# Kernel tuning notes

Hardware: AMD Instinct MI355X
Metric: run time of the kernel (lower is better)

## Reference

```python
import jax, jax.numpy as jnp
import numpy as np

B, S, H, E, K = 4, 4096, 2048, 64, 2
LN_EPS = 1e-5
AUX_EPS = 1e-9


def setup_inputs() -> dict:
    key = jax.random.key(0)
    ks = jax.random.split(key, 5)
    lim1 = 1.0 / np.sqrt(H)
    x = jax.random.normal(ks[0], (B, S, H), dtype=jnp.float32)
    W1 = jax.random.uniform(ks[1], (H, H), jnp.float32, -lim1, lim1)
    b1 = jax.random.uniform(ks[2], (H,), jnp.float32, -lim1, lim1)
    W2 = jax.random.uniform(ks[3], (H, E), jnp.float32, -lim1, lim1)
    b2 = jax.random.uniform(ks[4], (E,), jnp.float32, -lim1, lim1)
    gamma = jnp.ones((H,), jnp.float32)
    beta = jnp.zeros((H,), jnp.float32)
    return {"x": x, "W1": W1, "b1": b1, "W2": W2, "b2": b2, "gamma": gamma, "beta": beta}


def reference(x, W1, b1, W2, b2, gamma, beta):
    # LayerNorm over hidden dim
    mu = jnp.mean(x, axis=-1, keepdims=True)
    var = jnp.mean(jnp.square(x - mu), axis=-1, keepdims=True)
    x_norm = (x - mu) * jax.lax.rsqrt(var + LN_EPS) * gamma + beta
    # 2-layer router MLP: Linear -> ReLU -> Linear
    h = jax.nn.relu(jnp.einsum('bsh,hk->bsk', x_norm, W1) + b1)
    logits = jnp.einsum('bsh,he->bse', h, W2) + b2  # [B,S,E]
    probs = jax.nn.softmax(logits, axis=-1)
    # top-k + renormalize
    top_k_probs, top_k_indices = jax.lax.top_k(probs, K)
    top_k_probs = top_k_probs / jnp.sum(top_k_probs, axis=-1, keepdims=True)
    # aux load-balancing loss
    p_expert = jnp.mean(probs, axis=(0, 1))  # [E]
    aux_loss = jnp.sum(p_expert * jnp.log(p_expert * E + AUX_EPS))
    return top_k_indices, top_k_probs, aux_loss
```

## Files before the change

### kernel.cpp

```cpp
#include <hip/hip_runtime.h>
#include <hip/hip_fp16.h>
#include <cstdint>
#include <cstddef>

#define HH   2048
#define MM   16384
#define NE   64
#define FIXCAP 3072
#define MARGIN 1.0e-3f
#define LN_EPS  1e-5f
#define AUX_EPS 1e-9f

typedef __attribute__((ext_vector_type(8))) _Float16 f16x8;
typedef __attribute__((ext_vector_type(4))) _Float16 f16x4;
typedef __attribute__((ext_vector_type(4))) float    f32x4;

__device__ __forceinline__ void gload_lds16(const void* g, void* l) {
    __builtin_amdgcn_global_load_lds(
        (const __attribute__((address_space(1))) unsigned int*)g,
        (__attribute__((address_space(3))) unsigned int*)l,
        16, 0, 0);
}

__device__ __forceinline__ uint32_t swz64(uint32_t x) {
    return x ^ (((x >> 7) & 3u) << 4) ^ (((x >> 9) & 1u) << 6);
}
__device__ __forceinline__ uint32_t swz128(uint32_t x) {
    return x ^ (((x >> 8) & 7u) << 4);
}

__global__ __launch_bounds__(256) void k_tw1(const float* __restrict__ W1,
                                             _Float16* __restrict__ whp,
                                             _Float16* __restrict__ wlp) {
    __shared__ float tile[32][33];
    int tx = threadIdx.x & 31;
    int ty = threadIdx.x >> 5;
    int bx = blockIdx.x & 63;
    int by = blockIdx.x >> 6;
#pragma unroll
    for (int i = 0; i < 4; ++i) {
        int k = by * 32 + ty + i * 8;
        tile[ty + i * 8][tx] = W1[(size_t)k * HH + bx * 32 + tx];
    }
    __syncthreads();
#pragma unroll
    for (int i = 0; i < 4; ++i) {
        int n = bx * 32 + ty + i * 8;
        float w = tile[tx][ty + i * 8];
        _Float16 hi = (_Float16)w;
        _Float16 lo = (_Float16)((w - (float)hi) * 1024.0f);
        whp[(size_t)n * HH + by * 32 + tx] = hi;
        wlp[(size_t)n * HH + by * 32 + tx] = lo;
    }
}

__global__ __launch_bounds__(256) void k_w2q(const float* __restrict__ W2,
                                             _Float16* __restrict__ w2q) {
    int e = blockIdx.x;
    int t = threadIdx.x;
#pragma unroll
    for (int j = 0; j < 8; ++j) {
        int c = t * 8 + j;
        float w = W2[(size_t)c * NE + e];
        _Float16 hi = (_Float16)w;
        _Float16 lo = (_Float16)((w - (float)hi) * 1024.0f);
        f16x4 q = {hi, hi, lo, (_Float16)0.0f};
        *(f16x4*)&w2q[(size_t)e * 8192 + (size_t)c * 4] = q;
    }
}

__global__ __launch_bounds__(256) void k_ln(const float* __restrict__ x,
                                            const float* __restrict__ gamma,
                                            const float* __restrict__ beta,
                                            _Float16* __restrict__ xh,
                                            _Float16* __restrict__ xl) {
    int row = blockIdx.x;
    int t = threadIdx.x;
    const float4* xr = (const float4*)(x + (size_t)row * HH);
    float4 v0 = xr[t];
    float4 v1 = xr[t + 256];
    float s  = v0.x + v0.y + v0.z + v0.w + v1.x + v1.y + v1.z + v1.w;
    float sq = v0.x*v0.x + v0.y*v0.y + v0.z*v0.z + v0.w*v0.w
             + v1.x*v1.x + v1.y*v1.y + v1.z*v1.z + v1.w*v1.w;
#pragma unroll
    for (int m = 1; m < 64; m <<= 1) { s += __shfl_xor(s, m); sq += __shfl_xor(sq, m); }
    __shared__ float red[8];
    int wv = t >> 6;
    if ((t & 63) == 0) { red[wv] = s; red[wv + 4] = sq; }
    __syncthreads();
    s  = red[0] + red[1] + red[2] + red[3];
    sq = red[4] + red[5] + red[6] + red[7];
    float mu  = s * (1.0f / HH);
    float var = sq * (1.0f / HH) - mu * mu;
    float rr  = rsqrtf(var + LN_EPS);

    const float4* gr = (const float4*)gamma;
    const float4* br = (const float4*)beta;
#pragma unroll
    for (int p = 0; p < 2; ++p) {
        int idx = t + p * 256;
        float4 v = (p == 0) ? v0 : v1;
        float4 g = gr[idx];
        float4 b = br[idx];
        float f[4];
        f[0] = (v.x - mu) * rr * g.x + b.x;
        f[1] = (v.y - mu) * rr * g.y + b.y;
        f[2] = (v.z - mu) * rr * g.z + b.z;
        f[3] = (v.w - mu) * rr * g.w + b.w;
        f16x4 oh, ol;
#pragma unroll
        for (int j = 0; j < 4; ++j) {
            _Float16 hi = (_Float16)f[j];
            oh[j] = hi;
            ol[j] = (_Float16)(f[j] - (float)hi);
        }
        *(f16x4*)&xh[(size_t)row * HH + idx * 4] = oh;
        *(f16x4*)&xl[(size_t)row * HH + idx * 4] = ol;
    }
}

#define VMW0 do { asm volatile("s_waitcnt vmcnt(0)" ::: "memory"); \
                  __builtin_amdgcn_sched_barrier(0); } while (0)

#define STAGE1(IT) do { uint32_t kb = (uint32_t)(IT) * 128;                    \
    char* dst = lds + (((IT) & 1) << 16);                                      \
    gload_lds16(pxh + gA0 + kb,      dst + dstb0);                             \
    gload_lds16(pxh + gA1 + kb,      dst + dstb1);                             \
    gload_lds16(pxh + gA0 + kb + 64, dst + 16384 + dstb0);                     \
    gload_lds16(pxh + gA1 + kb + 64, dst + 16384 + dstb1);                     \
    gload_lds16(pwh + gB0 + kb,      dst + 32768 + dstb0);                     \
    gload_lds16(pwh + gB1 + kb,      dst + 32768 + dstb1);                     \
    gload_lds16(pwh + gB0 + kb + 64, dst + 49152 + dstb0);                     \
    gload_lds16(pwh + gB1 + kb + 64, dst + 49152 + dstb1);                     \
} while (0)

__global__ __launch_bounds__(512, 2) void k_gemm1(const _Float16* __restrict__ Ah_g,
                                                  const _Float16* __restrict__ Bh_g,
                                                  const _Float16* __restrict__ w2q,
                                                  const float* __restrict__ b1,
                                                  float* __restrict__ part) {
    __shared__ __align__(16) char lds[131072];

    int xcd = blockIdx.x & 7;
    int idx = blockIdx.x >> 3;
    int bm  = xcd * 8 + (idx >> 3);
    int bn  = idx & 7;
    int t = threadIdx.x;
    int lane = t & 63;
    int wid = t >> 6;
    int wm = wid >> 2;
    int wn = wid & 3;
    int r16 = lane & 15, ko = lane >> 4;

    f32x4 acc[8][4];
#pragma unroll
    for (int m = 0; m < 8; ++m)
#pragma unroll
        for (int n = 0; n < 4; ++n)
            acc[m][n] = (f32x4){0.f, 0.f, 0.f, 0.f};

    const char* pxh = (const char*)Ah_g;
    const char* pwh = (const char*)Bh_g;

    uint32_t dstb0 = (uint32_t)t * 16;
    uint32_t dstb1 = 8192 + dstb0;
    uint32_t L0 = swz64(dstb0), L1 = swz64(dstb1);
    uint32_t gA0 = ((uint32_t)bm * 256 + (L0 >> 6)) * (HH * 2) + (L0 & 63);
    uint32_t gA1 = ((uint32_t)bm * 256 + (L1 >> 6)) * (HH * 2) + (L1 & 63);
    uint32_t gB0 = ((uint32_t)bn * 256 + (L0 >> 6)) * (HH * 2) + (L0 & 63);
    uint32_t gB1 = ((uint32_t)bn * 256 + (L1 >> 6)) * (HH * 2) + (L1 & 63);

    uint32_t aoff[8], boff[4];
#pragma unroll
    for (int m = 0; m < 8; ++m)
        aoff[m] = swz64((uint32_t)(wm * 128 + m * 16 + r16) * 64 + ko * 16);
#pragma unroll
    for (int n = 0; n < 4; ++n)
        boff[n] = swz64((uint32_t)(wn * 64 + n * 16 + r16) * 64 + ko * 16);

    STAGE1(0);
    VMW0;
    __builtin_amdgcn_s_barrier();

    for (int it = 0; it < 32; ++it) {
        char* slot = lds + ((it & 1) << 16);
#pragma unroll
        for (int sub = 0; sub < 2; ++sub) {
            const char* Axh = slot + sub * 16384;
            const char* Bwh = slot + 32768 + sub * 16384;
            f16x8 fbh[4], fah[4];
#pragma unroll
            for (int n = 0; n < 4; ++n) fbh[n] = *(const f16x8*)(Bwh + boff[n]);
#pragma unroll
            for (int m = 0; m < 4; ++m) fah[m] = *(const f16x8*)(Axh + aoff[m]);
            if (sub == 0 && it < 31) STAGE1(it + 1);
            __builtin_amdgcn_s_setprio(1);
#pragma unroll
            for (int m = 0; m < 4; ++m)
#pragma unroll
                for (int n = 0; n < 4; ++n)
                    acc[m][n] = __builtin_amdgcn_mfma_f32_16x16x32_f16(fah[m], fbh[n], acc[m][n], 0, 0, 0);
            __builtin_amdgcn_s_setprio(0);
#pragma unroll
            for (int m = 0; m < 4; ++m) fah[m] = *(const f16x8*)(Axh + aoff[4 + m]);
            __builtin_amdgcn_s_setprio(1);
#pragma unroll
            for (int m = 0; m < 4; ++m)
#pragma unroll
                for (int n = 0; n < 4; ++n)
                    acc[4 + m][n] = __builtin_amdgcn_mfma_f32_16x16x32_f16(fah[m], fbh[n], acc[4 + m][n], 0, 0, 0);
            __builtin_amdgcn_s_setprio(0);
        }
        if (it < 31) VMW0;
        __builtin_amdgcn_s_barrier();
    }

    char* A2 = lds;
    char* B2 = lds + 32768;

    float bv[4];
#pragma unroll
    for (int n = 0; n < 4; ++n)
        bv[n] = b1[bn * 256 + wn * 64 + n * 16 + r16];

    f32x4 acc2[2][4];
#pragma unroll
    for (int mf = 0; mf < 2; ++mf)
#pragma unroll
        for (int ef = 0; ef < 4; ++ef)
            acc2[mf][ef] = (f32x4){0.f, 0.f, 0.f, 0.f};

    int hi4 = lane >> 4;
    int ko16 = ko * 16;

#pragma unroll
    for (int c = 0; c < 16; ++c) {
        {
            int e = t >> 3;
            int cb = (t & 7) * 16;
            const char* src = (const char*)w2q + (size_t)e * 16384
                            + (size_t)bn * 2048 + (size_t)c * 128 + cb;
            *(f16x8*)(B2 + swz128((uint32_t)e * 128 + cb)) = *(const f16x8*)src;
        }
        if (wn == (c >> 2)) {
            const int n = c & 3;
#pragma unroll
            for (int m = 0; m < 8; ++m)
#pragma unroll
                for (int i = 0; i < 4; ++i) {
                    float h = acc[m][n][i] + bv[n];
                    h = fmaxf(h, 0.f);
                    _Float16 hh = (_Float16)h;
                    float hhf = (float)hh;
                    _Float16 hl = (_Float16)(h - hhf);
                    _Float16 hs = (_Float16)(hhf * 0.0009765625f);
                    int row = wm * 128 + m * 16 + hi4 * 4 + i;
                    f16x4 q = {hh, hl, hs, (_Float16)0.0f};
                    *(f16x4*)(A2 + swz128((uint32_t)row * 128 + r16 * 8)) = q;
                }
        }
        __syncthreads();
#pragma unroll
        for (int kk = 0; kk < 2; ++kk) {
            f16x8 bfr[4];
#pragma unroll
            for (int ef = 0; ef < 4; ++ef)
                bfr[ef] = *(const f16x8*)(B2 +
                    swz128((uint32_t)(ef * 16 + r16) * 128 + kk * 64 + ko16));
#pragma unroll
            for (int mf = 0; mf < 2; ++mf) {
                f16x8 afr = *(const f16x8*)(A2 +
                    swz128((uint32_t)(wid * 32 + mf * 16 + r16) * 128 + kk * 64 + ko16));
#pragma unroll
                for (int ef = 0; ef < 4; ++ef)
                    acc2[mf][ef] = __builtin_amdgcn_mfma_f32_16x16x32_f16(
                        afr, bfr[ef], acc2[mf][ef], 0, 0, 0);
            }
        }
        __syncthreads();
    }

#pragma unroll
    for (int mf = 0; mf < 2; ++mf)
#pragma unroll
        for (int i = 0; i < 4; ++i) {
            int grow = bm * 256 + wid * 32 + mf * 16 + hi4 * 4 + i;
            float* dst = part + ((size_t)bn * MM + grow) * NE;
#pragma unroll
            for (int ef = 0; ef < 4; ++ef)
                dst[ef * 16 + r16] = acc2[mf][ef][i];
        }
}

__global__ __launch_bounds__(64) void k_screen(const float* __restrict__ part,
                                               const float* __restrict__ b2,
                                               float* __restrict__ out,
                                               float* __restrict__ sums,
                                               int* __restrict__ list,
                                               int* __restrict__ cnt) {
    int lane = threadIdx.x;
    int r = blockIdx.x * 64 + lane;
    float l[NE];
#pragma unroll
    for (int e = 0; e < NE; e += 4) {
        float4 b = *(const float4*)&b2[e];
        l[e] = b.x; l[e + 1] = b.y; l[e + 2] = b.z; l[e + 3] = b.w;
    }
    for (int sl = 0; sl < 8; ++sl) {
        const float* ps = part + ((size_t)sl * MM + r) * NE;
#pragma unroll
        for (int e = 0; e < NE; e += 4) {
            float4 v = *(const float4*)&ps[e];
            l[e] += v.x; l[e + 1] += v.y; l[e + 2] += v.z; l[e + 3] += v.w;
        }
    }
    float m1 = -1e30f, m2 = -1e30f, m3 = -1e30f;
    int i1 = 0, i2 = 0;
#pragma unroll
    for (int e = 0; e < NE; ++e) {
        if (l[e] > m1)      { m3 = m2; m2 = m1; i2 = i1; m1 = l[e]; i1 = e; }
        else if (l[e] > m2) { m3 = m2; m2 = l[e]; i2 = e; }
        else if (l[e] > m3) { m3 = l[e]; }
    }
    float ev[NE];
    float Z = 0.f;
#pragma unroll
    for (int e = 0; e < NE; ++e) { ev[e] = expf(l[e] - m1); Z += ev[e]; }

    float eb = expf(m2 - m1);
    float pa = 1.0f / (1.0f + eb);
    float pb = eb * pa;

    out[(size_t)r * 2 + 0] = (float)i1;
    out[(size_t)r * 2 + 1] = (float)i2;
    out[(size_t)2 * MM + r * 2 + 0] = pa;
    out[(size_t)2 * MM + r * 2 + 1] = pb;

    if ((m1 - m2 < MARGIN) || (m2 - m3 < MARGIN)) {
        int s = atomicAdd(cnt, 1);
        if (s < FIXCAP) list[s] = r;
    }

    float invZ = 1.0f / Z;
    float keep = 0.f;
#pragma unroll
    for (int e = 0; e < NE; ++e) {
        float q = ev[e] * invZ;
#pragma unroll
        for (int sh = 1; sh < 64; sh <<= 1) q += __shfl_xor(q, sh);
        if (lane == e) keep = q;
    }
    atomicAdd(&sums[lane], keep);
}

#define STAGEF_A(KT) do { uint32_t kb = (uint32_t)(KT) * 64;                   \
    char* dst = lds + (((KT) & 1) << 16);                                      \
    gload_lds16(pxh + gA0 + kb, dst + dstb0);                                  \
    gload_lds16(pxh + gA1 + kb, dst + dstb1);                                  \
    gload_lds16(pxl + gA0 + kb, dst + 16384 + dstb0);                          \
    gload_lds16(pxl + gA1 + kb, dst + 16384 + dstb1);                          \
} while (0)

#define STAGEF_B(KT) do { uint32_t kb = (uint32_t)(KT) * 64;                   \
    char* dst = lds + (((KT) & 1) << 16) + 32768;                              \
    gload_lds16(pwh + gB0 + kb, dst + dstb0);                                  \
    gload_lds16(pwh + gB1 + kb, dst + dstb1);                                  \
    gload_lds16(pwl + gB0 + kb, dst + 16384 + dstb0);                          \
    gload_lds16(pwl + gB1 + kb, dst + 16384 + dstb1);                          \
} while (0)

__global__ __launch_bounds__(512, 2) void k_fixg(const _Float16* __restrict__ Ah_g,
                                                 const _Float16* __restrict__ Al_g,
                                                 const _Float16* __restrict__ Bh_g,
                                                 const _Float16* __restrict__ Bl_g,
                                                 const int* __restrict__ list,
                                                 const int* __restrict__ cnt,
                                                 float* __restrict__ hpart) {
    int ks = blockIdx.x & 3;
    int bn = (blockIdx.x >> 2) & 7;
    int bm = blockIdx.x >> 5;
    int cv = *cnt; if (cv > FIXCAP) cv = FIXCAP;
    if (bm * 256 >= cv) return;

    __shared__ __align__(16) char lds[131072];
    int t = threadIdx.x;
    int lane = t & 63;
    int wid = t >> 6;
    int wm = wid >> 2;
    int wn = wid & 3;
    int r16 = lane & 15, ko = lane >> 4;

    f32x4 acc[8][4];
#pragma unroll
    for (int m = 0; m < 8; ++m)
#pragma unroll
        for (int n = 0; n < 4; ++n)
            acc[m][n] = (f32x4){0.f, 0.f, 0.f, 0.f};

    const char* pxh = (const char*)Ah_g;
    const char* pxl = (const char*)Al_g;
    const char* pwh = (const char*)Bh_g;
    const char* pwl = (const char*)Bl_g;

    uint32_t dstb0 = (uint32_t)t * 16;
    uint32_t dstb1 = 8192 + dstb0;
    uint32_t L0 = swz64(dstb0), L1 = swz64(dstb1);
    int rA0 = list[bm * 256 + (L0 >> 6)];
    int rA1 = list[bm * 256 + (L1 >> 6)];
    uint32_t kso = (uint32_t)ks * 1024;
    uint32_t gA0 = (uint32_t)rA0 * (HH * 2) + (L0 & 63) + kso;
    uint32_t gA1 = (uint32_t)rA1 * (HH * 2) + (L1 & 63) + kso;
    uint32_t gB0 = ((uint32_t)bn * 256 + (L0 >> 6)) * (HH * 2) + (L0 & 63) + kso;
    uint32_t gB1 = ((uint32_t)bn * 256 + (L1 >> 6)) * (HH * 2) + (L1 & 63) + kso;

    uint32_t aoff[8], boff[4];
#pragma unroll
    for (int m = 0; m < 8; ++m)
        aoff[m] = swz64((uint32_t)(wm * 128 + m * 16 + r16) * 64 + ko * 16);
#pragma unroll
    for (int n = 0; n < 4; ++n)
        boff[n] = swz64((uint32_t)(wn * 64 + n * 16 + r16) * 64 + ko * 16);

    STAGEF_A(0);
    STAGEF_B(0);
    VMW0;
    __builtin_amdgcn_s_barrier();

    for (int kt = 0; kt < 16; ++kt) {
        char* slot = lds + ((kt & 1) << 16);
        const char* Axh = slot;
        const char* Axl = slot + 16384;
        const char* Bwh = slot + 32768;
        const char* Bwl = slot + 49152;

        f16x8 fbh[4], fbl[4], fah[4], fal[4];
#pragma unroll
        for (int n = 0; n < 4; ++n) {
            fbh[n] = *(const f16x8*)(Bwh + boff[n]);
            fbl[n] = *(const f16x8*)(Bwl + boff[n]);
        }
#pragma unroll
        for (int m = 0; m < 4; ++m) {
            fah[m] = *(const f16x8*)(Axh + aoff[m]);
            fal[m] = *(const f16x8*)(Axl + aoff[m]);
        }
        if (kt < 15) STAGEF_A(kt + 1);
        __builtin_amdgcn_s_setprio(1);
#pragma unroll
        for (int m = 0; m < 4; ++m) {
            f16x8 fas = fah[m] * (_Float16)0.0009765625f;
#pragma unroll
            for (int n = 0; n < 4; ++n) {
                acc[m][n] = __builtin_amdgcn_mfma_f32_16x16x32_f16(fah[m], fbh[n], acc[m][n], 0, 0, 0);
                acc[m][n] = __builtin_amdgcn_mfma_f32_16x16x32_f16(fal[m], fbh[n], acc[m][n], 0, 0, 0);
                acc[m][n] = __builtin_amdgcn_mfma_f32_16x16x32_f16(fas,    fbl[n], acc[m][n], 0, 0, 0);
            }
        }
        __builtin_amdgcn_s_setprio(0);

#pragma unroll
        for (int m = 0; m < 4; ++m) {
            fah[m] = *(const f16x8*)(Axh + aoff[4 + m]);
            fal[m] = *(const f16x8*)(Axl + aoff[4 + m]);
        }
        if (kt < 15) STAGEF_B(kt + 1);
        __builtin_amdgcn_s_setprio(1);
#pragma unroll
        for (int m = 0; m < 4; ++m) {
            f16x8 fas = fah[m] * (_Float16)0.0009765625f;
#pragma unroll
            for (int n = 0; n < 4; ++n) {
                acc[4 + m][n] = __builtin_amdgcn_mfma_f32_16x16x32_f16(fah[m], fbh[n], acc[4 + m][n], 0, 0, 0);
                acc[4 + m][n] = __builtin_amdgcn_mfma_f32_16x16x32_f16(fal[m], fbh[n], acc[4 + m][n], 0, 0, 0);
                acc[4 + m][n] = __builtin_amdgcn_mfma_f32_16x16x32_f16(fas,    fbl[n], acc[4 + m][n], 0, 0, 0);
            }
        }
        __builtin_amdgcn_s_setprio(0);
        if (kt < 15) VMW0;
        __builtin_amdgcn_s_barrier();
    }

    float* hp = hpart + (size_t)ks * FIXCAP * HH;
    int hi4 = lane >> 4;
#pragma unroll
    for (int m = 0; m < 8; ++m)
#pragma unroll
        for (int n = 0; n < 4; ++n)
#pragma unroll
            for (int i = 0; i < 4; ++i) {
                int row_l = bm * 256 + wm * 128 + m * 16 + hi4 * 4 + i;
                int col = bn * 256 + wn * 64 + n * 16 + r16;
                hp[(size_t)row_l * HH + col] = acc[m][n][i];
            }
}

__global__ __launch_bounds__(256) void k_fix2(const float* __restrict__ hpart,
                                              const float* __restrict__ b1,
                                              const float* __restrict__ W2,
                                              const float* __restrict__ b2,
                                              const int* __restrict__ list,
                                              const int* __restrict__ cnt,
                                              float* __restrict__ out) {
    int n = *cnt; if (n > FIXCAP) n = FIXCAP;
    int gi = blockIdx.x;
    if (gi >= n) return;
    int r = list[gi];
    int e = threadIdx.x & 63;
    int kg = threadIdx.x >> 6;
    const float* h0 = hpart + (size_t)gi * HH;
    const float* h1 = h0 + (size_t)FIXCAP * HH;
    const float* h2 = h1 + (size_t)FIXCAP * HH;
    const float* h3 = h2 + (size_t)FIXCAP * HH;
    float p = 0.f;
    int k0 = kg * 512;
    for (int k = k0; k < k0 + 512; ++k) {
        float h = ((h0[k] + h1[k]) + (h2[k] + h3[k])) + b1[k];
        h = fmaxf(h, 0.f);
        p = fmaf(h, W2[(size_t)k * NE + e], p);
    }
    __shared__ float red[4][NE];
    red[kg][e] = p;
    __syncthreads();
    if (threadIdx.x < 64) {
        float l = ((red[0][e] + red[1][e]) + (red[2][e] + red[3][e])) + b2[e];
        float m1 = l;
#pragma unroll
        for (int sh = 1; sh < 64; sh <<= 1) m1 = fmaxf(m1, __shfl_xor(m1, sh));
        unsigned long long bb = __ballot(l == m1);
        int i1 = (int)(__ffsll((long long)bb) - 1);
        float l2 = (e == i1) ? -1e30f : l;
        float m2 = l2;
#pragma unroll
        for (int sh = 1; sh < 64; sh <<= 1) m2 = fmaxf(m2, __shfl_xor(m2, sh));
        unsigned long long bb2 = __ballot(l2 == m2);
        int i2 = (int)(__ffsll((long long)bb2) - 1);
        if (e == 0) {
            float eb = expf(m2 - m1);
            float pa = 1.0f / (1.0f + eb);
            float pb = eb * pa;
            out[(size_t)r * 2 + 0] = (float)i1;
            out[(size_t)r * 2 + 1] = (float)i2;
            out[(size_t)2 * MM + r * 2 + 0] = pa;
            out[(size_t)2 * MM + r * 2 + 1] = pb;
        }
    }
}

__global__ void k_aux(const float* __restrict__ sums, float* __restrict__ out) {
    if (threadIdx.x == 0) {
        float loss = 0.f;
        for (int e = 0; e < NE; ++e) {
            float p = sums[e] * (1.0f / MM);
            loss += p * logf(p * (float)NE + AUX_EPS);
        }
        out[(size_t)4 * MM] = loss;
    }
}

extern "C" void kernel_launch(void* const* d_in, const int* in_sizes, int n_in,
                              void* d_out, int out_size, void* d_ws, size_t ws_size,
                              hipStream_t stream) {
    const float* x     = (const float*)d_in[0];
    const float* W1    = (const float*)d_in[1];
    const float* b1    = (const float*)d_in[2];
    const float* W2    = (const float*)d_in[3];
    const float* b2    = (const float*)d_in[4];
    const float* gamma = (const float*)d_in[5];
    const float* beta  = (const float*)d_in[6];
    float* out = (float*)d_out;

    char* ws = (char*)d_ws;
    _Float16* xh   = (_Float16*)(ws);
    _Float16* xl   = (_Float16*)(ws + 67108864);
    _Float16* whp  = (_Float16*)(ws + 134217728);
    _Float16* wlp  = (_Float16*)(ws + 142606336);
    _Float16* w2q  = (_Float16*)(ws + 150994944);
    float*    part = (float*)   (ws + 152043520);
    float*   hpart = (float*)   (ws + 152043520);
    int*      list = (int*)     (ws + 252706816);
    float*    sums = (float*)   (ws + 252719104);
    int*      cnt  = (int*)     (ws + 252719360);

    hipMemsetAsync(sums, 0, 512, stream);
    hipMemsetAsync(list, 0, FIXCAP * 4, stream);
    k_tw1   <<<4096,    256, 0, stream>>>(W1, whp, wlp);
    k_w2q   <<<64,      256, 0, stream>>>(W2, w2q);
    k_ln    <<<MM,      256, 0, stream>>>(x, gamma, beta, xh, xl);
    k_gemm1 <<<512,     512, 0, stream>>>(xh, whp, w2q, b1, part);
    k_screen<<<MM/64,   64,  0, stream>>>(part, b2, out, sums, list, cnt);
    k_fixg  <<<384,     512, 0, stream>>>(xh, xl, whp, wlp, list, cnt, hpart);
    k_fix2  <<<FIXCAP,  256, 0, stream>>>(hpart, b1, W2, b2, list, cnt, out);
    k_aux   <<<1,       64,  0, stream>>>(sums, out);
}
```

Measured before the change: 367.7 us.

## Deepen GEMM1 LDS pipeline to four stages and use one wavefront per row in LayerNorm

The main GEMM loop moves from a double-buffered 128-wide K step to a four-slot ring of 64-wide K steps with three tiles in flight. It waits with partial vmcnt counts, so each step no longer has to fully drain outstanding loads before its barrier, which is meant to hide global-to-LDS latency better. Separately, the LayerNorm kernel now handles one row per wavefront, four rows per block, which drops the LDS reduction and block barrier. The trade-off is twice as many barriers in GEMM1 and more VGPRs in LayerNorm to hold eight float4 values per lane.

```diff
diff --git a/kernel.cpp b/kernel.cpp
--- a/kernel.cpp
+++ b/kernel.cpp
@@ -74,22 +74,19 @@
                                             const float* __restrict__ beta,
                                             _Float16* __restrict__ xh,
                                             _Float16* __restrict__ xl) {
-    int row = blockIdx.x;
-    int t = threadIdx.x;
+    int row = blockIdx.x * 4 + (threadIdx.x >> 6);
+    int lane = threadIdx.x & 63;
     const float4* xr = (const float4*)(x + (size_t)row * HH);
-    float4 v0 = xr[t];
-    float4 v1 = xr[t + 256];
-    float s  = v0.x + v0.y + v0.z + v0.w + v1.x + v1.y + v1.z + v1.w;
-    float sq = v0.x*v0.x + v0.y*v0.y + v0.z*v0.z + v0.w*v0.w
-             + v1.x*v1.x + v1.y*v1.y + v1.z*v1.z + v1.w*v1.w;
+    float4 v[8];
+    float s = 0.f, sq = 0.f;
+#pragma unroll
+    for (int j = 0; j < 8; ++j) {
+        v[j] = xr[lane + j * 64];
+        s  += v[j].x + v[j].y + v[j].z + v[j].w;
+        sq += v[j].x*v[j].x + v[j].y*v[j].y + v[j].z*v[j].z + v[j].w*v[j].w;
+    }
 #pragma unroll
     for (int m = 1; m < 64; m <<= 1) { s += __shfl_xor(s, m); sq += __shfl_xor(sq, m); }
-    __shared__ float red[8];
-    int wv = t >> 6;
-    if ((t & 63) == 0) { red[wv] = s; red[wv + 4] = sq; }
-    __syncthreads();
-    s  = red[0] + red[1] + red[2] + red[3];
-    sq = red[4] + red[5] + red[6] + red[7];
     float mu  = s * (1.0f / HH);
     float var = sq * (1.0f / HH) - mu * mu;
     float rr  = rsqrtf(var + LN_EPS);
@@ -97,41 +94,36 @@
     const float4* gr = (const float4*)gamma;
     const float4* br = (const float4*)beta;
 #pragma unroll
-    for (int p = 0; p < 2; ++p) {
-        int idx = t + p * 256;
-        float4 v = (p == 0) ? v0 : v1;
+    for (int j = 0; j < 8; ++j) {
+        int idx = lane + j * 64;
         float4 g = gr[idx];
         float4 b = br[idx];
         float f[4];
-        f[0] = (v.x - mu) * rr * g.x + b.x;
-        f[1] = (v.y - mu) * rr * g.y + b.y;
-        f[2] = (v.z - mu) * rr * g.z + b.z;
-        f[3] = (v.w - mu) * rr * g.w + b.w;
+        f[0] = (v[j].x - mu) * rr * g.x + b.x;
+        f[1] = (v[j].y - mu) * rr * g.y + b.y;
+        f[2] = (v[j].z - mu) * rr * g.z + b.z;
+        f[3] = (v[j].w - mu) * rr * g.w + b.w;
         f16x4 oh, ol;
 #pragma unroll
-        for (int j = 0; j < 4; ++j) {
-            _Float16 hi = (_Float16)f[j];
-            oh[j] = hi;
-            ol[j] = (_Float16)(f[j] - (float)hi);
+        for (int q = 0; q < 4; ++q) {
+            _Float16 hi = (_Float16)f[q];
+            oh[q] = hi;
+            ol[q] = (_Float16)(f[q] - (float)hi);
         }
         *(f16x4*)&xh[(size_t)row * HH + idx * 4] = oh;
         *(f16x4*)&xl[(size_t)row * HH + idx * 4] = ol;
     }
 }
 
-#define VMW0 do { asm volatile("s_waitcnt vmcnt(0)" ::: "memory"); \
-                  __builtin_amdgcn_sched_barrier(0); } while (0)
-
-#define STAGE1(IT) do { uint32_t kb = (uint32_t)(IT) * 128;                    \
-    char* dst = lds + (((IT) & 1) << 16);                                      \
-    gload_lds16(pxh + gA0 + kb,      dst + dstb0);                             \
-    gload_lds16(pxh + gA1 + kb,      dst + dstb1);                             \
-    gload_lds16(pxh + gA0 + kb + 64, dst + 16384 + dstb0);                     \
-    gload_lds16(pxh + gA1 + kb + 64, dst + 16384 + dstb1);                     \
-    gload_lds16(pwh + gB0 + kb,      dst + 32768 + dstb0);                     \
-    gload_lds16(pwh + gB1 + kb,      dst + 32768 + dstb1);                     \
-    gload_lds16(pwh + gB0 + kb + 64, dst + 49152 + dstb0);                     \
-    gload_lds16(pwh + gB1 + kb + 64, dst + 49152 + dstb1);                     \
+#define VMW(N) do { asm volatile("s_waitcnt vmcnt(" #N ")" ::: "memory"); \
+                    __builtin_amdgcn_sched_barrier(0); } while (0)
+
+#define STAGE1(KT) do { uint32_t kb = (uint32_t)(KT) * 64;                     \
+    char* dst = lds + (((KT) & 3) << 15);                                      \
+    gload_lds16(pxh + gA0 + kb, dst + dstb0);                                  \
+    gload_lds16(pxh + gA1 + kb, dst + dstb1);                                  \
+    gload_lds16(pwh + gB0 + kb, dst + 16384 + dstb0);                          \
+    gload_lds16(pwh + gB1 + kb, dst + 16384 + dstb1);                          \
 } while (0)
 
 __global__ __launch_bounds__(512, 2) void k_gemm1(const _Float16* __restrict__ Ah_g,
@@ -179,39 +171,41 @@
         boff[n] = swz64((uint32_t)(wn * 64 + n * 16 + r16) * 64 + ko * 16);
 
     STAGE1(0);
-    VMW0;
+    STAGE1(1);
+    STAGE1(2);
+    VMW(8);
     __builtin_amdgcn_s_barrier();
 
-    for (int it = 0; it < 32; ++it) {
-        char* slot = lds + ((it & 1) << 16);
-#pragma unroll
-        for (int sub = 0; sub < 2; ++sub) {
-            const char* Axh = slot + sub * 16384;
-            const char* Bwh = slot + 32768 + sub * 16384;
-            f16x8 fbh[4], fah[4];
-#pragma unroll
-            for (int n = 0; n < 4; ++n) fbh[n] = *(const f16x8*)(Bwh + boff[n]);
-#pragma unroll
-            for (int m = 0; m < 4; ++m) fah[m] = *(const f16x8*)(Axh + aoff[m]);
-            if (sub == 0 && it < 31) STAGE1(it + 1);
-            __builtin_amdgcn_s_setprio(1);
-#pragma unroll
-            for (int m = 0; m < 4; ++m)
-#pragma unroll
-                for (int n = 0; n < 4; ++n)
-                    acc[m][n] = __builtin_amdgcn_mfma_f32_16x16x32_f16(fah[m], fbh[n], acc[m][n], 0, 0, 0);
-            __builtin_amdgcn_s_setprio(0);
-#pragma unroll
-            for (int m = 0; m < 4; ++m) fah[m] = *(const f16x8*)(Axh + aoff[4 + m]);
-            __builtin_amdgcn_s_setprio(1);
-#pragma unroll
-            for (int m = 0; m < 4; ++m)
-#pragma unroll
-                for (int n = 0; n < 4; ++n)
-                    acc[4 + m][n] = __builtin_amdgcn_mfma_f32_16x16x32_f16(fah[m], fbh[n], acc[4 + m][n], 0, 0, 0);
-            __builtin_amdgcn_s_setprio(0);
-        }
-        if (it < 31) VMW0;
+    for (int kt = 0; kt < 64; ++kt) {
+        char* slot = lds + ((kt & 3) << 15);
+        const char* Axh = slot;
+        const char* Bwh = slot + 16384;
+
+        f16x8 fbh[4], fah[4];
+#pragma unroll
+        for (int n = 0; n < 4; ++n) fbh[n] = *(const f16x8*)(Bwh + boff[n]);
+#pragma unroll
+        for (int m = 0; m < 4; ++m) fah[m] = *(const f16x8*)(Axh + aoff[m]);
+        if (kt < 61) STAGE1(kt + 3);
+        __builtin_amdgcn_s_setprio(1);
+#pragma unroll
+        for (int m = 0; m < 4; ++m)
+#pragma unroll
+            for (int n = 0; n < 4; ++n)
+                acc[m][n] = __builtin_amdgcn_mfma_f32_16x16x32_f16(fah[m], fbh[n], acc[m][n], 0, 0, 0);
+        __builtin_amdgcn_s_setprio(0);
+#pragma unroll
+        for (int m = 0; m < 4; ++m) fah[m] = *(const f16x8*)(Axh + aoff[4 + m]);
+        __builtin_amdgcn_s_setprio(1);
+#pragma unroll
+        for (int m = 0; m < 4; ++m)
+#pragma unroll
+            for (int n = 0; n < 4; ++n)
+                acc[4 + m][n] = __builtin_amdgcn_mfma_f32_16x16x32_f16(fah[m], fbh[n], acc[4 + m][n], 0, 0, 0);
+        __builtin_amdgcn_s_setprio(0);
+        if (kt < 61)      VMW(8);
+        else if (kt == 61) VMW(4);
+        else if (kt == 62) VMW(0);
         __builtin_amdgcn_s_barrier();
     }
 
@@ -352,6 +346,9 @@
     }
     atomicAdd(&sums[lane], keep);
 }
+
+#define VMW0 do { asm volatile("s_waitcnt vmcnt(0)" ::: "memory"); \
+                  __builtin_amdgcn_sched_barrier(0); } while (0)
 
 #define STAGEF_A(KT) do { uint32_t kb = (uint32_t)(KT) * 64;                   \
     char* dst = lds + (((KT) & 1) << 16);                                      \
@@ -585,7 +582,7 @@
     hipMemsetAsync(list, 0, FIXCAP * 4, stream);
     k_tw1   <<<4096,    256, 0, stream>>>(W1, whp, wlp);
     k_w2q   <<<64,      256, 0, stream>>>(W2, w2q);
-    k_ln    <<<MM,      256, 0, stream>>>(x, gamma, beta, xh, xl);
+    k_ln    <<<MM/4,    256, 0, stream>>>(x, gamma, beta, xh, xl);
     k_gemm1 <<<512,     512, 0, stream>>>(xh, whp, w2q, b1, part);
     k_screen<<<MM/64,   64,  0, stream>>>(part, b2, out, sums, list, cnt);
     k_fixg  <<<384,     512, 0, stream>>>(xh, xl, whp, wlp, list, cnt, hpart);
```

Measured after the change: 368.5 us. About the same (+0.2%).
